# Performance work log

Measured on AMD Instinct MI355X. Metric: run time of the kernel, lower is better.

## Reference

```python
import jax, jax.numpy as jnp
import numpy as np

B, N, D, H, DH, E, BIAS_DIM = 8, 512, 512, 8, 64, 32768, 8

def setup_inputs() -> dict:
    key = jax.random.key(0)
    ks = jax.random.split(key, 10)
    states = jax.random.normal(ks[0], (B, N, D), jnp.float32)
    key_states = jax.random.normal(ks[1], (B, N, D), jnp.float32)
    # causal mask, broadcastable over heads: [B,1,N,N]
    masks = jnp.broadcast_to(jnp.tril(jnp.ones((N, N), jnp.float32)), (B, 1, N, N))
    edge_type = jax.random.randint(ks[2], (E, 1), 0, BIAS_DIM, jnp.int32)
    b_idx = jax.random.randint(ks[3], (E, 1), 0, B, jnp.int32)
    q_idx = jax.random.randint(ks[4], (E, 1), 0, N, jnp.int32)
    k_idx = jax.random.randint(ks[5], (E, 1), 0, N, jnp.int32)
    attention_bias = jnp.concatenate([edge_type, b_idx, q_idx, k_idx], axis=1)
    s = 0.05
    Wq = jax.random.normal(ks[6], (D, H, DH), jnp.float32) * s
    Wk = jax.random.normal(ks[7], (D, H, DH), jnp.float32) * s
    Wv = jax.random.normal(ks[8], (D, H, DH), jnp.float32) * s
    k2 = jax.random.split(ks[9], 3)
    Wo = jax.random.normal(k2[0], (H, DH, D), jnp.float32) * s
    bias_embs = jax.random.normal(k2[1], (BIAS_DIM, DH), jnp.float32) * s
    bias_scalar = jax.random.normal(k2[2], (DH, 1), jnp.float32) * s
    return {"states": states, "key_states": key_states, "masks": masks,
            "attention_bias": attention_bias, "Wq": Wq, "Wk": Wk, "Wv": Wv,
            "Wo": Wo, "bias_embs": bias_embs, "bias_scalar": bias_scalar}

def reference(states, key_states, masks, attention_bias, Wq, Wk, Wv, Wo, bias_embs, bias_scalar):
    q = jnp.einsum('btd,dha->btha', states, Wq)
    k = jnp.einsum('btd,dha->btha', key_states, Wk)
    v = jnp.einsum('btd,dha->btha', key_states, Wv)
    alpha = jnp.einsum('bkha,bqha->bhqk', k, q)  # [B,H,Q,K]
    # sparse edge bias: embed edge types, project to scalar, scatter into [B,Q,K]
    et = attention_bias[:, 0]
    bias_vals = (bias_embs[et] @ bias_scalar)[:, 0]  # [E]
    bq, bk = alpha.shape[2], alpha.shape[3]
    bias_mat = jnp.zeros((alpha.shape[0], bq, bk), alpha.dtype)
    bias_mat = bias_mat.at[attention_bias[:, 1], attention_bias[:, 2], attention_bias[:, 3]].add(bias_vals)
    summed_keys = jnp.sum(k, axis=-1)  # [B,K,H]
    alpha = alpha + jnp.einsum('bqk,bkh->bhqk', bias_mat, summed_keys)
    alpha = alpha * jax.lax.rsqrt(jnp.float32(DH))
    neg = jnp.finfo(jnp.float32).min
    alpha = alpha * masks + (1.0 - jnp.ceil(masks)) * neg
    alpha = jax.nn.softmax(alpha, axis=-1)
    alpha = alpha * masks
    context = jnp.einsum('bhqk,bkha->bqha', alpha, v)
    return jnp.einsum('btha,had->btd', context, Wo)
```

## Files before the change

kernel.cpp:

```cpp
#include <hip/hip_runtime.h>

typedef unsigned short u16;
typedef unsigned int u32;
typedef __bf16 bf16x8 __attribute__((ext_vector_type(8)));
typedef float f32x4 __attribute__((ext_vector_type(4)));
typedef u16 u16x8 __attribute__((ext_vector_type(8)));
typedef u16 u16x4 __attribute__((ext_vector_type(4)));


__device__ __forceinline__ u16 f2b(float f) {
  union { float f; u32 i; } v; v.f = f;
  u32 r = v.i + 0x7fffu + ((v.i >> 16) & 1u);
  return (u16)(r >> 16);
}
__device__ __forceinline__ float b2f(u16 u) {
  union { u32 i; float f; } v; v.i = ((u32)u) << 16; return v.f;
}

__global__ __launch_bounds__(256) void prologue(
    const float* __restrict__ states, const float* __restrict__ key_states,
    const float* __restrict__ Wq, const float* __restrict__ Wk,
    const float* __restrict__ Wv, const float* __restrict__ Wo,
    const int* __restrict__ ab, const float* __restrict__ be,
    const float* __restrict__ bsc,
    u16* __restrict__ sb, u16* __restrict__ kbin, u16* __restrict__ wbase,
    float* __restrict__ bias_mat, int n_edges) {
  __shared__ u16 t[32][33];
  __shared__ float tv[8];
  int bid = blockIdx.x;
  int tid = threadIdx.x;
  if (bid < 2048) {
    const float* src = (bid >= 1024) ? key_states : states;
    u16* dst = (bid >= 1024) ? kbin : sb;
    int gid = (bid & 1023) * 256 + tid;
    const float4* sp = (const float4*)src + (size_t)gid * 2;
    float4 x0 = sp[0], x1 = sp[1];
    u16x8 p;
    p[0] = f2b(x0.x); p[1] = f2b(x0.y); p[2] = f2b(x0.z); p[3] = f2b(x0.w);
    p[4] = f2b(x1.x); p[5] = f2b(x1.y); p[6] = f2b(x1.z); p[7] = f2b(x1.w);
    *(u16x8*)(dst + (size_t)gid * 8) = p;
  } else if (bid < 3072) {
    int tt = bid - 2048;
    int z = tt >> 8, rem = tt & 255;
    int bx = rem & 15, by = rem >> 4;
    const float* src; float sc = 1.f;
    if (z == 0)      { src = Wq; sc = 0.125f; }
    else if (z == 1) { src = Wk; }
    else if (z == 2) { src = Wv; }
    else             { src = Wo; }
    u16* dst = wbase + (size_t)z * 262144;
    int tx = tid & 31, ty = tid >> 5;
    int c0 = bx * 32, r0 = by * 32;
    #pragma unroll
    for (int i = ty; i < 32; i += 8) t[i][tx] = f2b(src[(r0 + i) * 512 + c0 + tx] * sc);
    __syncthreads();
    #pragma unroll
    for (int i = ty; i < 32; i += 8) dst[(c0 + i) * 512 + r0 + tx] = t[tx][i];
  } else {
    if (tid < 8) {
      float s = 0.f;
      #pragma unroll
      for (int a = 0; a < 64; a++) s += be[tid * 64 + a] * bsc[a];
      tv[tid] = s * 0.125f;
    }
    __syncthreads();
    int e = (bid - 3072) * 256 + tid;
    if (e < n_edges) {
      int et = ab[e * 4 + 0];
      int b  = ab[e * 4 + 1];
      int qi = ab[e * 4 + 2];
      int ki = ab[e * 4 + 3];
      atomicAdd(&bias_mat[((size_t)b * 512 + qi) * 512 + ki], tv[et]);
    }
  }
}

__global__ __launch_bounds__(256) void qkv_gemm(const u16* __restrict__ sb,
                                                const u16* __restrict__ kbin,
                                                const u16* __restrict__ wT,
                                                u16* __restrict__ qb,
                                                u16* __restrict__ kbo,
                                                u16* __restrict__ vtb) {
  __shared__ u16 As[64 * 72];
  __shared__ u16 Bs[128 * 72];
  int tid = threadIdx.x;
  int lane = tid & 63, wave = tid >> 6;
  int quad = lane >> 4, ln = lane & 15;
  int row0 = blockIdx.x * 64;
  int col0 = blockIdx.y * 128;
  const u16* A = (col0 < 512) ? sb : kbin;
  int ara = tid >> 2, aca = (tid & 3) * 16;
  int arb = tid >> 1, acb = (tid & 1) * 32;

  f32x4 acc[4][2];
  #pragma unroll
  for (int i = 0; i < 4; i++)
    #pragma unroll
    for (int j = 0; j < 2; j++) acc[i][j] = (f32x4){0.f, 0.f, 0.f, 0.f};

  const u16* ap = A + (size_t)(row0 + ara) * 512 + aca;
  const u16* bp = wT + (size_t)(col0 + arb) * 512 + acb;

  u16x8 ra0, ra1, rb0, rb1, rb2, rb3;
  ra0 = *(const u16x8*)(ap + 0);  ra1 = *(const u16x8*)(ap + 8);
  rb0 = *(const u16x8*)(bp + 0);  rb1 = *(const u16x8*)(bp + 8);
  rb2 = *(const u16x8*)(bp + 16); rb3 = *(const u16x8*)(bp + 24);

  for (int k0 = 0; k0 < 512; k0 += 64) {
    __syncthreads();
    *(u16x8*)&As[ara * 72 + aca + 0] = ra0;  *(u16x8*)&As[ara * 72 + aca + 8] = ra1;
    *(u16x8*)&Bs[arb * 72 + acb + 0]  = rb0;  *(u16x8*)&Bs[arb * 72 + acb + 8]  = rb1;
    *(u16x8*)&Bs[arb * 72 + acb + 16] = rb2;  *(u16x8*)&Bs[arb * 72 + acb + 24] = rb3;
    __syncthreads();
    if (k0 < 448) {
      int kn = k0 + 64;
      ra0 = *(const u16x8*)(ap + kn + 0);  ra1 = *(const u16x8*)(ap + kn + 8);
      rb0 = *(const u16x8*)(bp + kn + 0);  rb1 = *(const u16x8*)(bp + kn + 8);
      rb2 = *(const u16x8*)(bp + kn + 16); rb3 = *(const u16x8*)(bp + kn + 24);
    }
    #pragma unroll
    for (int s = 0; s < 2; s++) {
      bf16x8 af[4], bfv[2];
      #pragma unroll
      for (int i = 0; i < 4; i++)
        af[i] = *(bf16x8*)&As[(i * 16 + ln) * 72 + s * 32 + quad * 8];
      #pragma unroll
      for (int j = 0; j < 2; j++)
        bfv[j] = *(bf16x8*)&Bs[(wave * 32 + j * 16 + ln) * 72 + s * 32 + quad * 8];
      #pragma unroll
      for (int i = 0; i < 4; i++)
        #pragma unroll
        for (int j = 0; j < 2; j++)
          acc[i][j] = __builtin_amdgcn_mfma_f32_16x16x32_bf16(af[i], bfv[j], acc[i][j], 0, 0, 0);
    }
  }

  int region = col0 >> 9;
  int nbase = col0 & 511;
  if (region <= 1) {
    u16* Cout = region ? kbo : qb;
    #pragma unroll
    for (int i = 0; i < 4; i++)
      #pragma unroll
      for (int j = 0; j < 2; j++) {
        int mb = row0 + i * 16 + quad * 4;
        int n = nbase + wave * 32 + j * 16 + ln;
        #pragma unroll
        for (int r = 0; r < 4; r++)
          Cout[(size_t)(mb + r) * 512 + n] = f2b(acc[i][j][r]);
      }
  } else {
    #pragma unroll
    for (int i = 0; i < 4; i++)
      #pragma unroll
      for (int j = 0; j < 2; j++) {
        int mb = row0 + i * 16 + quad * 4;
        int bb = mb >> 9, t0 = mb & 511;
        int a_abs = nbase + wave * 32 + j * 16 + ln;
        int h = a_abs >> 6, a = a_abs & 63;
        u16x4 p;
        p[0] = f2b(acc[i][j][0]); p[1] = f2b(acc[i][j][1]);
        p[2] = f2b(acc[i][j][2]); p[3] = f2b(acc[i][j][3]);
        *(u16x4*)&vtb[(((size_t)bb * 8 + h) * 64 + a) * 512 + t0] = p;
      }
  }
}

__global__ __launch_bounds__(256) void out_gemm(const u16* __restrict__ A,
                                                const u16* __restrict__ BT,
                                                float* __restrict__ C) {
  __shared__ u16 As[64 * 72];
  __shared__ u16 Bs[64 * 72];
  int tid = threadIdx.x;
  int lane = tid & 63, wave = tid >> 6;
  int quad = lane >> 4, ln = lane & 15;
  int wr = wave >> 1, wc = wave & 1;
  int row0 = blockIdx.x * 64;
  int col0 = blockIdx.y * 64;
  int ar = tid >> 2, ac = (tid & 3) * 16;

  f32x4 acc[2][2];
  #pragma unroll
  for (int i = 0; i < 2; i++)
    #pragma unroll
    for (int j = 0; j < 2; j++) acc[i][j] = (f32x4){0.f, 0.f, 0.f, 0.f};

  const u16* ap = A + (size_t)(row0 + ar) * 512 + ac;
  const u16* bp = BT + (size_t)(col0 + ar) * 512 + ac;

  u16x8 ra0, ra1, rb0, rb1;
  ra0 = *(const u16x8*)(ap + 0); ra1 = *(const u16x8*)(ap + 8);
  rb0 = *(const u16x8*)(bp + 0); rb1 = *(const u16x8*)(bp + 8);

  for (int k0 = 0; k0 < 512; k0 += 64) {
    __syncthreads();
    *(u16x8*)&As[ar * 72 + ac + 0] = ra0;  *(u16x8*)&As[ar * 72 + ac + 8] = ra1;
    *(u16x8*)&Bs[ar * 72 + ac + 0] = rb0;  *(u16x8*)&Bs[ar * 72 + ac + 8] = rb1;
    __syncthreads();
    if (k0 < 448) {
      int kn = k0 + 64;
      ra0 = *(const u16x8*)(ap + kn + 0); ra1 = *(const u16x8*)(ap + kn + 8);
      rb0 = *(const u16x8*)(bp + kn + 0); rb1 = *(const u16x8*)(bp + kn + 8);
    }
    #pragma unroll
    for (int s = 0; s < 2; s++) {
      bf16x8 af[2], bfv[2];
      #pragma unroll
      for (int i = 0; i < 2; i++)
        af[i] = *(bf16x8*)&As[(wr * 32 + i * 16 + ln) * 72 + s * 32 + quad * 8];
      #pragma unroll
      for (int j = 0; j < 2; j++)
        bfv[j] = *(bf16x8*)&Bs[(wc * 32 + j * 16 + ln) * 72 + s * 32 + quad * 8];
      #pragma unroll
      for (int i = 0; i < 2; i++)
        #pragma unroll
        for (int j = 0; j < 2; j++)
          acc[i][j] = __builtin_amdgcn_mfma_f32_16x16x32_bf16(af[i], bfv[j], acc[i][j], 0, 0, 0);
    }
  }
  #pragma unroll
  for (int i = 0; i < 2; i++)
    #pragma unroll
    for (int j = 0; j < 2; j++) {
      int mb = row0 + wr * 32 + i * 16 + quad * 4;
      int n = col0 + wc * 32 + j * 16 + ln;
      #pragma unroll
      for (int r = 0; r < 4; r++)
        C[(size_t)(mb + r) * 512 + n] = acc[i][j][r];
    }
}

__global__ __launch_bounds__(256) void sumk2(const u16* __restrict__ k,
                                             float* __restrict__ summed) {
  int gid = blockIdx.x * 256 + threadIdx.x;
  int group = gid >> 3;
  int b = group >> 12, rem = group & 4095;
  int t = rem >> 3, h = rem & 7;
  int j = gid & 7;
  u16x8 x = *(const u16x8*)(k + ((size_t)(b * 512 + t)) * 512 + h * 64 + j * 8);
  float s = 0.f;
  #pragma unroll
  for (int e = 0; e < 8; e++) s += b2f(x[e]);
  s += __shfl_xor(s, 1);
  s += __shfl_xor(s, 2);
  s += __shfl_xor(s, 4);
  if (j == 0) summed[(b * 8 + h) * 512 + t] = s;
}

__global__ __launch_bounds__(256) void attn_mfma(const u16* __restrict__ q,
                                                 const u16* __restrict__ k,
                                                 const u16* __restrict__ vt,
                                                 const float* __restrict__ bias_mat,
                                                 const float* __restrict__ summed,
                                                 u16* __restrict__ ctx,
                                                 float* __restrict__ Opart,
                                                 float* __restrict__ ml) {
  __shared__ u16 Qs[64 * 72];
  __shared__ u16 Ks[64 * 72];
  __shared__ u16 Vt[64 * 72];
  __shared__ u16 Ps[4][16 * 72];
  int tid = threadIdx.x;
  int wave = tid >> 6, lane = tid & 63;
  int quad = lane >> 4, ln = lane & 15;
  int blk = blockIdx.x;
  int bh = blk / 12;
  int u = blk - bh * 12;
  int b = bh >> 3, h = bh & 7;
  int qt, kb0, kbe, part = 0;
  bool partial;
  if (u < 4) { qt = u; kb0 = 0; kbe = u; partial = false; }
  else {
    int v = u - 4; qt = 4 + (v >> 1); part = v & 1; partial = true;
    if (part == 0) { kb0 = 0; kbe = 3; } else { kb0 = 4; kbe = qt; }
  }
  int q0 = qt * 64;

  int sr = tid >> 2;
  int sc2 = (tid & 3) * 16;

  {
    const u16* qp = q + ((size_t)(b * 512 + q0 + sr)) * 512 + h * 64 + sc2;
    *(u16x8*)&Qs[sr * 72 + sc2] = *(const u16x8*)qp;
    *(u16x8*)&Qs[sr * 72 + sc2 + 8] = *(const u16x8*)(qp + 8);
  }

  float m_r[4], l_r[4];
  f32x4 o[4];
  #pragma unroll
  for (int r = 0; r < 4; r++) { m_r[r] = -3.40282347e38f; l_r[r] = 0.f; }
  #pragma unroll
  for (int nt = 0; nt < 4; nt++) o[nt] = (f32x4){0.f, 0.f, 0.f, 0.f};

  const u16* kp0 = k + ((size_t)(b * 512 + sr)) * 512 + h * 64 + sc2;
  const u16* vp0 = vt + ((size_t)(bh * 64 + sr)) * 512 + sc2;

  u16x8 rk0 = *(const u16x8*)(kp0 + (size_t)kb0 * 64 * 512);
  u16x8 rk1 = *(const u16x8*)(kp0 + (size_t)kb0 * 64 * 512 + 8);
  u16x8 rv0 = *(const u16x8*)(vp0 + kb0 * 64);
  u16x8 rv1 = *(const u16x8*)(vp0 + kb0 * 64 + 8);

  int qrow = q0 + wave * 16 + quad * 4;

  float c_skv[4], c_bias[4][4];
  #pragma unroll
  for (int nt = 0; nt < 4; nt++) {
    int t = kb0 * 64 + nt * 16 + ln;
    c_skv[nt] = summed[bh * 512 + t];
    const float* bp2 = bias_mat + ((size_t)(b * 512 + qrow)) * 512 + t;
    #pragma unroll
    for (int r = 0; r < 4; r++) c_bias[nt][r] = bp2[(size_t)r * 512];
  }

  for (int kb = kb0; kb <= kbe; kb++) {
    __syncthreads();
    *(u16x8*)&Ks[sr * 72 + sc2] = rk0;
    *(u16x8*)&Ks[sr * 72 + sc2 + 8] = rk1;
    *(u16x8*)&Vt[sr * 72 + sc2] = rv0;
    *(u16x8*)&Vt[sr * 72 + sc2 + 8] = rv1;
    __syncthreads();

    float n_skv[4], n_bias[4][4];
    if (kb < kbe) {
      const u16* kp = kp0 + (size_t)(kb + 1) * 64 * 512;
      const u16* vp = vp0 + (kb + 1) * 64;
      rk0 = *(const u16x8*)kp;
      rk1 = *(const u16x8*)(kp + 8);
      rv0 = *(const u16x8*)vp;
      rv1 = *(const u16x8*)(vp + 8);
      #pragma unroll
      for (int nt = 0; nt < 4; nt++) {
        int t = (kb + 1) * 64 + nt * 16 + ln;
        n_skv[nt] = summed[bh * 512 + t];
        const float* bp2 = bias_mat + ((size_t)(b * 512 + qrow)) * 512 + t;
        #pragma unroll
        for (int r = 0; r < 4; r++) n_bias[nt][r] = bp2[(size_t)r * 512];
      }
    }

    bf16x8 aq0 = *(bf16x8*)&Qs[(wave * 16 + ln) * 72 + quad * 8];
    bf16x8 aq1 = *(bf16x8*)&Qs[(wave * 16 + ln) * 72 + 32 + quad * 8];
    f32x4 s[4];
    #pragma unroll
    for (int nt = 0; nt < 4; nt++) {
      bf16x8 b0 = *(bf16x8*)&Ks[(nt * 16 + ln) * 72 + quad * 8];
      bf16x8 b1 = *(bf16x8*)&Ks[(nt * 16 + ln) * 72 + 32 + quad * 8];
      s[nt] = (f32x4){0.f, 0.f, 0.f, 0.f};
      s[nt] = __builtin_amdgcn_mfma_f32_16x16x32_bf16(aq0, b0, s[nt], 0, 0, 0);
      s[nt] = __builtin_amdgcn_mfma_f32_16x16x32_bf16(aq1, b1, s[nt], 0, 0, 0);
    }

    #pragma unroll
    for (int nt = 0; nt < 4; nt++) {
      int t = kb * 64 + nt * 16 + ln;
      #pragma unroll
      for (int r = 0; r < 4; r++) {
        float val = s[nt][r] + c_bias[nt][r] * c_skv[nt];
        s[nt][r] = (t <= qrow + r) ? val : -3.40282347e38f;
      }
    }

    float alpha[4];
    #pragma unroll
    for (int r = 0; r < 4; r++) {
      float tm = fmaxf(fmaxf(s[0][r], s[1][r]), fmaxf(s[2][r], s[3][r]));
      #pragma unroll
      for (int off = 8; off; off >>= 1) tm = fmaxf(tm, __shfl_xor(tm, off));
      float mn = fmaxf(m_r[r], tm);
      alpha[r] = __expf(m_r[r] - mn);
      m_r[r] = mn;
      float rs = 0.f;
      #pragma unroll
      for (int nt = 0; nt < 4; nt++) {
        float pp = __expf(s[nt][r] - mn);
        s[nt][r] = pp;
        rs += pp;
      }
      #pragma unroll
      for (int off = 8; off; off >>= 1) rs += __shfl_xor(rs, off);
      l_r[r] = l_r[r] * alpha[r] + rs;
    }

    #pragma unroll
    for (int nt = 0; nt < 4; nt++)
      #pragma unroll
      for (int r = 0; r < 4; r++)
        Ps[wave][(quad * 4 + r) * 72 + nt * 16 + ln] = f2b(s[nt][r]);
    #pragma unroll
    for (int nt = 0; nt < 4; nt++)
      #pragma unroll
      for (int r = 0; r < 4; r++)
        o[nt][r] *= alpha[r];

    bf16x8 ap0 = *(bf16x8*)&Ps[wave][ln * 72 + quad * 8];
    bf16x8 ap1 = *(bf16x8*)&Ps[wave][ln * 72 + 32 + quad * 8];
    #pragma unroll
    for (int nt = 0; nt < 4; nt++) {
      bf16x8 b0 = *(bf16x8*)&Vt[(nt * 16 + ln) * 72 + quad * 8];
      bf16x8 b1 = *(bf16x8*)&Vt[(nt * 16 + ln) * 72 + 32 + quad * 8];
      o[nt] = __builtin_amdgcn_mfma_f32_16x16x32_bf16(ap0, b0, o[nt], 0, 0, 0);
      o[nt] = __builtin_amdgcn_mfma_f32_16x16x32_bf16(ap1, b1, o[nt], 0, 0, 0);
    }

    if (kb < kbe) {
      #pragma unroll
      for (int nt = 0; nt < 4; nt++) {
        c_skv[nt] = n_skv[nt];
        #pragma unroll
        for (int r = 0; r < 4; r++) c_bias[nt][r] = n_bias[nt][r];
      }
    }
  }

  if (!partial) {
    #pragma unroll
    for (int r = 0; r < 4; r++) {
      float inv = 1.f / l_r[r];
      int qr2 = qrow + r;
      u16* dst = ctx + ((size_t)(b * 512 + qr2)) * 512 + h * 64;
      #pragma unroll
      for (int nt = 0; nt < 4; nt++)
        dst[nt * 16 + ln] = f2b(o[nt][r] * inv);
    }
  } else {
    #pragma unroll
    for (int r = 0; r < 4; r++) {
      int row = qrow + r - 256;
      float* dst = Opart + (((size_t)(part * 64 + bh)) * 256 + row) * 64;
      #pragma unroll
      for (int nt = 0; nt < 4; nt++)
        dst[nt * 16 + ln] = o[nt][r];
    }
    if (ln == 0) {
      #pragma unroll
      for (int r = 0; r < 4; r++) {
        int row = qrow + r - 256;
        float* mp = ml + (((size_t)(part * 64 + bh)) * 256 + row) * 2;
        mp[0] = m_r[r];
        mp[1] = l_r[r];
      }
    }
  }
}

__global__ __launch_bounds__(256) void attn_merge(const float* __restrict__ Opart,
                                                  const float* __restrict__ ml,
                                                  u16* __restrict__ ctx) {
  int gid = blockIdx.x * 256 + threadIdx.x;
  int col = gid & 63;
  int row = (gid >> 6) & 255;
  int bh = gid >> 14;
  size_t i0 = (size_t)bh * 256 + row;
  size_t i1 = (size_t)(64 + bh) * 256 + row;
  float m0 = ml[i0 * 2], l0 = ml[i0 * 2 + 1];
  float m1 = ml[i1 * 2], l1 = ml[i1 * 2 + 1];
  float m = fmaxf(m0, m1);
  float a0 = __expf(m0 - m), a1 = __expf(m1 - m);
  float l = l0 * a0 + l1 * a1;
  float O0 = Opart[i0 * 64 + col], O1 = Opart[i1 * 64 + col];
  float val = (O0 * a0 + O1 * a1) / l;
  int b = bh >> 3, h = bh & 7, qrow = 256 + row;
  ctx[((size_t)(b * 512 + qrow)) * 512 + h * 64 + col] = f2b(val);
}

extern "C" void kernel_launch(void* const* d_in, const int* in_sizes, int n_in,
                              void* d_out, int out_size, void* d_ws, size_t ws_size,
                              hipStream_t stream) {
  const float* states     = (const float*)d_in[0];
  const float* key_states = (const float*)d_in[1];
  const int*   ab         = (const int*)d_in[3];
  const float* Wq         = (const float*)d_in[4];
  const float* Wk         = (const float*)d_in[5];
  const float* Wv         = (const float*)d_in[6];
  const float* Wo         = (const float*)d_in[7];
  const float* be         = (const float*)d_in[8];
  const float* bsc        = (const float*)d_in[9];
  float* out = (float*)d_out;

  char* ws = (char*)d_ws;
  const size_t MB = 1024 * 1024;
  u16* wbase    = (u16*)(ws);
  u16* wot      = (u16*)(ws + 1536 * 1024);
  u16* sb       = (u16*)(ws + 2 * MB);
  u16* kbin     = (u16*)(ws + 6 * MB);
  u16* qb       = (u16*)(ws + 10 * MB);
  u16* kbo      = (u16*)(ws + 14 * MB);
  u16* vtb      = (u16*)(ws + 18 * MB);
  u16* ctxb     = (u16*)(ws + 22 * MB);
  float* bias_m = (float*)(ws + 26 * MB);
  float* summed = (float*)(ws + 34 * MB);
  float* Opart  = (float*)(ws + 35 * MB);
  float* mlbuf  = (float*)(ws + 43 * MB);

  int n_edges = in_sizes[3] / 4;

  hipMemsetAsync(bias_m, 0, (size_t)8 * MB, stream);
  prologue<<<dim3(3072 + (n_edges + 255) / 256), 256, 0, stream>>>(
      states, key_states, Wq, Wk, Wv, Wo, ab, be, bsc, sb, kbin, wbase, bias_m, n_edges);
  qkv_gemm<<<dim3(64, 12), 256, 0, stream>>>(sb, kbin, wbase, qb, kbo, vtb);
  sumk2<<<dim3(1024), 256, 0, stream>>>(kbo, summed);
  attn_mfma<<<dim3(768), 256, 0, stream>>>(qb, kbo, vtb, bias_m, summed, ctxb, Opart, mlbuf);
  attn_merge<<<dim3(4096), 256, 0, stream>>>(Opart, mlbuf, ctxb);
  out_gemm<<<dim3(64, 8), 256, 0, stream>>>(ctxb, wot, out);
}
```

Before: 139.3 us.

## Fuse key-sum into QKV GEMM epilogue and reorder attention block scheduling

The per-head key sums are now computed inside the QKV GEMM epilogue from fp32 accumulators using lane shuffles and a small shared buffer, so the separate sumk2 kernel launch and its re-read of K are gone. The attention kernel also remaps block indices so that the heaviest work units (those covering the most key blocks) are dispatched first, with lighter ones after, to reduce tail imbalance. The fused sum uses fp32 accumulators rather than bf16-rounded K, which changes the numerics slightly. It also adds a __syncthreads inside a branch that every thread of the block takes uniformly.

```diff
diff --git a/kernel.cpp b/kernel.cpp
--- a/kernel.cpp
+++ b/kernel.cpp
@@ -80,9 +80,11 @@
                                                 const u16* __restrict__ wT,
                                                 u16* __restrict__ qb,
                                                 u16* __restrict__ kbo,
-                                                u16* __restrict__ vtb) {
+                                                u16* __restrict__ vtb,
+                                                float* __restrict__ summed) {
   __shared__ u16 As[64 * 72];
   __shared__ u16 Bs[128 * 72];
+  __shared__ float ssum[4][64];
   int tid = threadIdx.x;
   int lane = tid & 63, wave = tid >> 6;
   int quad = lane >> 4, ln = lane & 15;
@@ -149,6 +151,28 @@
         for (int r = 0; r < 4; r++)
           Cout[(size_t)(mb + r) * 512 + n] = f2b(acc[i][j][r]);
       }
+    if (region == 1) {
+      #pragma unroll
+      for (int i = 0; i < 4; i++)
+        #pragma unroll
+        for (int r = 0; r < 4; r++) {
+          float v = acc[i][0][r] + acc[i][1][r];
+          v += __shfl_xor(v, 1);
+          v += __shfl_xor(v, 2);
+          v += __shfl_xor(v, 4);
+          v += __shfl_xor(v, 8);
+          if (ln == 0) ssum[wave][i * 16 + quad * 4 + r] = v;
+        }
+      __syncthreads();
+      if (tid < 128) {
+        int hl = tid >> 6, row = tid & 63;
+        float s = ssum[hl * 2][row] + ssum[hl * 2 + 1][row];
+        int m = row0 + row;
+        int b = m >> 9, t = m & 511;
+        int h = (nbase >> 6) + hl;
+        summed[((size_t)(b * 8 + h)) * 512 + t] = s;
+      }
+    }
   } else {
     #pragma unroll
     for (int i = 0; i < 4; i++)
@@ -228,23 +252,6 @@
       for (int r = 0; r < 4; r++)
         C[(size_t)(mb + r) * 512 + n] = acc[i][j][r];
     }
-}
-
-__global__ __launch_bounds__(256) void sumk2(const u16* __restrict__ k,
-                                             float* __restrict__ summed) {
-  int gid = blockIdx.x * 256 + threadIdx.x;
-  int group = gid >> 3;
-  int b = group >> 12, rem = group & 4095;
-  int t = rem >> 3, h = rem & 7;
-  int j = gid & 7;
-  u16x8 x = *(const u16x8*)(k + ((size_t)(b * 512 + t)) * 512 + h * 64 + j * 8);
-  float s = 0.f;
-  #pragma unroll
-  for (int e = 0; e < 8; e++) s += b2f(x[e]);
-  s += __shfl_xor(s, 1);
-  s += __shfl_xor(s, 2);
-  s += __shfl_xor(s, 4);
-  if (j == 0) summed[(b * 8 + h) * 512 + t] = s;
 }
 
 __global__ __launch_bounds__(256) void attn_mfma(const u16* __restrict__ q,
@@ -262,9 +269,18 @@
   int tid = threadIdx.x;
   int wave = tid >> 6, lane = tid & 63;
   int quad = lane >> 4, ln = lane & 15;
-  int blk = blockIdx.x;
-  int bh = blk / 12;
-  int u = blk - bh * 12;
+  int p2 = blockIdx.x;
+  int bh, u;
+  {
+    const int fours[6] = {3, 4, 6, 8, 10, 11};
+    const int threes[2] = {2, 9};
+    const int ones[2] = {0, 5};
+    const int twos[2] = {1, 7};
+    if (p2 < 384)      { bh = p2 & 63; u = fours[p2 >> 6]; }
+    else if (p2 < 512) { int q2 = p2 - 384; bh = q2 & 63; u = threes[q2 >> 6]; }
+    else if (p2 < 640) { int q2 = p2 - 512; bh = q2 & 63; u = ones[q2 >> 6]; }
+    else               { int q2 = p2 - 640; bh = q2 & 63; u = twos[q2 >> 6]; }
+  }
   int b = bh >> 3, h = bh & 7;
   int qt, kb0, kbe, part = 0;
   bool partial;
@@ -496,8 +512,7 @@
   hipMemsetAsync(bias_m, 0, (size_t)8 * MB, stream);
   prologue<<<dim3(3072 + (n_edges + 255) / 256), 256, 0, stream>>>(
       states, key_states, Wq, Wk, Wv, Wo, ab, be, bsc, sb, kbin, wbase, bias_m, n_edges);
-  qkv_gemm<<<dim3(64, 12), 256, 0, stream>>>(sb, kbin, wbase, qb, kbo, vtb);
-  sumk2<<<dim3(1024), 256, 0, stream>>>(kbo, summed);
+  qkv_gemm<<<dim3(64, 12), 256, 0, stream>>>(sb, kbin, wbase, qb, kbo, vtb, summed);
   attn_mfma<<<dim3(768), 256, 0, stream>>>(qb, kbo, vtb, bias_m, summed, ctxb, Opart, mlbuf);
   attn_merge<<<dim3(4096), 256, 0, stream>>>(Opart, mlbuf, ctxb);
   out_gemm<<<dim3(64, 8), 256, 0, stream>>>(ctxb, wot, out);
```

Result: faster. 134.1 us (median of 2 runs) (-3.7%).
